# Kernel tuning notes

Measured on AMD Instinct MI355X. Metric: run time of the kernel, lower is better.

The kernel has to match this reference:

```python
import jax, jax.numpy as jnp
import numpy as np

OUT = 7            # output_size
SR = 2             # sampling_ratio
SCALES = (0.25, 0.125, 0.0625, 0.03125)  # P2..P5
CANON_S = 224.0
CANON_L = 4.0
LVL_EPS = 1e-6
K_MIN, K_MAX = 2, 5  # -log2(scales[0]), -log2(scales[-1])


def setup_inputs() -> dict:
    key = jax.random.key(0)
    ks = jax.random.split(key, 6)
    B, C, N = 2, 256, 256
    sizes = (200, 100, 50, 25)
    inp = {}
    for i, (k, hw) in enumerate(zip(ks[:4], sizes)):
        inp[f"feat{i}"] = jax.random.normal(k, (B, C, hw, hw), dtype=jnp.float32)
    x1y1 = jax.random.uniform(ks[4], (B, N, 2), minval=0.0, maxval=600.0)
    wh = jax.random.uniform(ks[5], (B, N, 2), minval=16.0, maxval=256.0)
    boxes = jnp.concatenate([x1y1, jnp.minimum(x1y1 + wh, 800.0)], axis=-1)
    inp["boxes"] = boxes.astype(jnp.float32)
    return inp


def _roi_align(feat, rois, scale):
    """torchvision RoIAlign (aligned=False). feat [B,C,H,W], rois [N,5] (bidx,x1,y1,x2,y2)."""
    B, C, H, W = feat.shape
    bidx = rois[:, 0].astype(jnp.int32)
    x1 = rois[:, 1] * scale
    y1 = rois[:, 2] * scale
    x2 = rois[:, 3] * scale
    y2 = rois[:, 4] * scale
    roi_w = jnp.maximum(x2 - x1, 1.0)
    roi_h = jnp.maximum(y2 - y1, 1.0)
    bin_h = roi_h / OUT
    bin_w = roi_w / OUT
    g = jnp.arange(OUT * SR)
    bin_idx = (g // SR).astype(feat.dtype)
    sub = (g % SR).astype(feat.dtype) + 0.5
    # sample coordinates [N, G] with G = OUT*SR
    ys = y1[:, None] + bin_idx * bin_h[:, None] + sub * bin_h[:, None] / SR
    xs = x1[:, None] + bin_idx * bin_w[:, None] + sub * bin_w[:, None] / SR
    vy = (ys >= -1.0) & (ys <= H)
    vx = (xs >= -1.0) & (xs <= W)
    y = jnp.clip(ys, 0.0, H - 1.0)
    x = jnp.clip(xs, 0.0, W - 1.0)
    y0 = jnp.floor(y).astype(jnp.int32)
    x0 = jnp.floor(x).astype(jnp.int32)
    y1i = jnp.minimum(y0 + 1, H - 1)
    x1i = jnp.minimum(x0 + 1, W - 1)
    ly = y - y0
    lx = x - x0
    hy = 1.0 - ly
    hx = 1.0 - lx

    def gather(yi, xi):
        # advanced indices at dims 0,2,3 with slice at dim 1 -> [N, G, G, C]
        return feat[bidx[:, None, None], :, yi[:, :, None], xi[:, None, :]]

    v = (gather(y0, x0) * (hy[:, :, None] * hx[:, None, :])[..., None]
         + gather(y0, x1i) * (hy[:, :, None] * lx[:, None, :])[..., None]
         + gather(y1i, x0) * (ly[:, :, None] * hx[:, None, :])[..., None]
         + gather(y1i, x1i) * (ly[:, :, None] * lx[:, None, :])[..., None])
    mask = (vy[:, :, None] & vx[:, None, :])[..., None]
    v = jnp.where(mask, v, 0.0)                       # [N, G, G, C]
    n = v.shape[0]
    v = v.reshape(n, OUT, SR, OUT, SR, C).mean(axis=(2, 4))  # avg pool per bin
    return jnp.transpose(v, (0, 3, 1, 2))             # [N, C, OUT, OUT]


def reference(feat0, feat1, feat2, feat3, boxes):
    feats = [feat0, feat1, feat2, feat3]
    B, N = boxes.shape[:2]
    flat = boxes.reshape(B * N, 4)
    ids = jnp.repeat(jnp.arange(B, dtype=flat.dtype), N)[:, None]
    rois = jnp.concatenate([ids, flat], axis=1)       # [B*N, 5]
    # FPN level assignment heuristic (LevelMapper)
    area = (flat[:, 2] - flat[:, 0]) * (flat[:, 3] - flat[:, 1])
    s = jnp.sqrt(area)
    lvl = jnp.floor(CANON_L + jnp.log2(s / CANON_S) + LVL_EPS)
    levels = jnp.clip(lvl, K_MIN, K_MAX).astype(jnp.int32) - K_MIN
    # Pool every roi at every level (static shapes), then select by level,
    # equivalent math to the gather/scatter-merge in the original.
    pooled = jnp.stack([_roi_align(f, rois, sc) for f, sc in zip(feats, SCALES)], axis=0)
    return pooled[levels, jnp.arange(B * N)]          # [B*N, C, OUT, OUT]
```

## Files before the change

### kernel.cpp

```cpp
#include <hip/hip_runtime.h>
#include <hip/hip_fp16.h>


#define ROI_OUT 7
#define NSAMP   14
#define C_TOT   256
#define N_PER_B 256
#define BINS    49
#define TOT_HW  53125

#define NTILE_X 832

__global__ __launch_bounds__(256)
void repack_kernel(const float* __restrict__ f0, const float* __restrict__ f1,
                   const float* __restrict__ f2, const float* __restrict__ f3,
                   __half* __restrict__ ws)
{
    __shared__ float tile[64][65];

    const int tx = blockIdx.x;
    const float* feat; int HW, base;
    int hw0;
    if (tx < 625)      { feat = f0; HW = 40000; base = 0;     hw0 = tx * 64; }
    else if (tx < 782) { feat = f1; HW = 10000; base = 40000; hw0 = (tx - 625) * 64; }
    else if (tx < 822) { feat = f2; HW = 2500;  base = 50000; hw0 = (tx - 782) * 64; }
    else               { feat = f3; HW = 625;   base = 52500; hw0 = (tx - 822) * 64; }

    const int c0 = blockIdx.y * 64;
    const int b  = blockIdx.z;
    const float* src = feat + (size_t)(b * C_TOT + c0) * (size_t)HW;

    const int hl  = threadIdx.x & 63;
    const int cl0 = threadIdx.x >> 6;
    const int hw  = hw0 + hl;
    if (hw < HW) {
        #pragma unroll
        for (int i = 0; i < 16; ++i) {
            int cl = cl0 + 4 * i;
            tile[cl][hl] = src[(size_t)cl * HW + hw];
        }
    }
    __syncthreads();

    __half* dst = ws + ((size_t)b * TOT_HW + base) * C_TOT + c0;
    const int co  = (threadIdx.x & 31) * 2;
    const int ho0 = threadIdx.x >> 5;
    #pragma unroll
    for (int i = 0; i < 8; ++i) {
        int ho  = ho0 + 8 * i;
        int hw2 = hw0 + ho;
        if (hw2 < HW) {
            __half2 v = __floats2half2_rn(tile[co][ho], tile[co + 1][ho]);
            *(__half2*)(dst + (size_t)hw2 * C_TOT + co) = v;
        }
    }
}

__global__ __launch_bounds__(256)
void msroi_main(const __half* __restrict__ ws, const float* __restrict__ boxes,
                float* __restrict__ out)
{
    __shared__ float oacc[C_TOT * BINS];
    __shared__ int4  pY[NSAMP], pX[NSAMP];

    const int tid = threadIdx.x;
    const int roi = blockIdx.x;
    const int b   = roi >> 8;

    const float* bxp = boxes + (size_t)roi * 4;
    float bx1 = bxp[0], by1 = bxp[1], bx2 = bxp[2], by2 = bxp[3];
    float area = (bx2 - bx1) * (by2 - by1);
    float s    = sqrtf(area);
    float lvlf = floorf(4.0f + log2f(s * (1.0f / 224.0f)) + 1e-6f);
    lvlf = fminf(fmaxf(lvlf, 2.0f), 5.0f);
    int level = (int)lvlf - 2;

    int H, W, lvbase; float scale;
    switch (level) {
        case 0:  H = 200; W = 200; lvbase = 0;     scale = 0.25f;    break;
        case 1:  H = 100; W = 100; lvbase = 40000; scale = 0.125f;   break;
        case 2:  H = 50;  W = 50;  lvbase = 50000; scale = 0.0625f;  break;
        default: H = 25;  W = 25;  lvbase = 52500; scale = 0.03125f; break;
    }

    float x1 = bx1 * scale, y1 = by1 * scale;
    float roi_w = fmaxf(bx2 * scale - x1, 1.0f);
    float roi_h = fmaxf(by2 * scale - y1, 1.0f);
    float bin_w = roi_w * (1.0f / ROI_OUT);
    float bin_h = roi_h * (1.0f / ROI_OUT);

    if (tid < 2 * NSAMP) {
        bool isy = tid >= NSAMP;
        int  j   = isy ? tid - NSAMP : tid;
        int  pb  = j >> 1, sub = j & 1;
        float start = isy ? y1 : x1;
        float bsz   = isy ? bin_h : bin_w;
        int   lim   = isy ? H : W;
        float ss = start + (float)pb * bsz + ((float)sub + 0.5f) * bsz * 0.5f;
        float v  = (ss >= -1.0f && ss <= (float)lim) ? 1.0f : 0.0f;
        float cc = fminf(fmaxf(ss, 0.0f), (float)lim - 1.0f);
        int   i0 = (int)floorf(cc);
        int   i1 = min(i0 + 1, lim - 1);
        float l  = cc - (float)i0;
        int4 pk; pk.x = i0; pk.y = i1;
        pk.z = __float_as_int(l); pk.w = __float_as_int(v);
        if (isy) pY[j] = pk; else pX[j] = pk;
    }
    __syncthreads();

    const int wave = tid >> 6;
    const int lane = tid & 63;
    const int c    = lane * 4;
    const __half* base = ws + ((size_t)b * TOT_HW + lvbase) * C_TOT + c;

    for (int bin = wave; bin < BINS; bin += 4) {
        int ph = bin / ROI_OUT;
        int pw = bin - ph * ROI_OUT;
        float a0 = 0.f, a1 = 0.f, a2 = 0.f, a3 = 0.f;

        #pragma unroll
        for (int sy = 0; sy < 2; ++sy) {
            int4 py  = pY[2 * ph + sy];
            float ly = __int_as_float(py.z);
            float vy = __int_as_float(py.w);
            float hy = 1.0f - ly;
            #pragma unroll
            for (int sx = 0; sx < 2; ++sx) {
                int4 px  = pX[2 * pw + sx];
                float lx = __int_as_float(px.z);
                float vv = vy * __int_as_float(px.w);
                float hx = 1.0f - lx;
                float w00 = vv * hy * hx, w01 = vv * hy * lx;
                float w10 = vv * ly * hx, w11 = vv * ly * lx;

                const __half2* p00 = (const __half2*)(base + (size_t)(py.x * W + px.x) * C_TOT);
                const __half2* p01 = (const __half2*)(base + (size_t)(py.x * W + px.y) * C_TOT);
                const __half2* p10 = (const __half2*)(base + (size_t)(py.y * W + px.x) * C_TOT);
                const __half2* p11 = (const __half2*)(base + (size_t)(py.y * W + px.y) * C_TOT);

                float2 g0, g1;
                g0 = __half22float2(p00[0]); g1 = __half22float2(p00[1]);
                a0 += w00 * g0.x; a1 += w00 * g0.y; a2 += w00 * g1.x; a3 += w00 * g1.y;
                g0 = __half22float2(p01[0]); g1 = __half22float2(p01[1]);
                a0 += w01 * g0.x; a1 += w01 * g0.y; a2 += w01 * g1.x; a3 += w01 * g1.y;
                g0 = __half22float2(p10[0]); g1 = __half22float2(p10[1]);
                a0 += w10 * g0.x; a1 += w10 * g0.y; a2 += w10 * g1.x; a3 += w10 * g1.y;
                g0 = __half22float2(p11[0]); g1 = __half22float2(p11[1]);
                a0 += w11 * g0.x; a1 += w11 * g0.y; a2 += w11 * g1.x; a3 += w11 * g1.y;
            }
        }
        oacc[(c + 0) * BINS + bin] = a0 * 0.25f;
        oacc[(c + 1) * BINS + bin] = a1 * 0.25f;
        oacc[(c + 2) * BINS + bin] = a2 * 0.25f;
        oacc[(c + 3) * BINS + bin] = a3 * 0.25f;
    }
    __syncthreads();

    float4*       o4 = (float4*)(out + (size_t)roi * (C_TOT * BINS));
    const float4* s4 = (const float4*)oacc;
    for (int j = tid; j < (C_TOT * BINS) / 4; j += 256) o4[j] = s4[j];
}

__global__ __launch_bounds__(256)
void msroi_direct(const float* __restrict__ f0, const float* __restrict__ f1,
                  const float* __restrict__ f2, const float* __restrict__ f3,
                  const float* __restrict__ boxes, float* __restrict__ out, int total)
{
    int e = blockIdx.x * 256 + threadIdx.x;
    if (e >= total) return;
    int bin = e % BINS;
    int c   = (e / BINS) % C_TOT;
    int roi = e / (BINS * C_TOT);
    int b   = roi / N_PER_B;

    const float* bx = boxes + (size_t)roi * 4;
    float bx1 = bx[0], by1 = bx[1], bx2 = bx[2], by2 = bx[3];
    float area = (bx2 - bx1) * (by2 - by1);
    float s    = sqrtf(area);
    float lvlf = floorf(4.0f + log2f(s * (1.0f / 224.0f)) + 1e-6f);
    lvlf = fminf(fmaxf(lvlf, 2.0f), 5.0f);
    int level = (int)lvlf - 2;

    const float* feat; int H, W; float scale;
    switch (level) {
        case 0:  feat = f0; H = 200; W = 200; scale = 0.25f;    break;
        case 1:  feat = f1; H = 100; W = 100; scale = 0.125f;   break;
        case 2:  feat = f2; H = 50;  W = 50;  scale = 0.0625f;  break;
        default: feat = f3; H = 25;  W = 25;  scale = 0.03125f; break;
    }
    float x1 = bx1 * scale, y1 = by1 * scale;
    float roi_w = fmaxf(bx2 * scale - x1, 1.0f);
    float roi_h = fmaxf(by2 * scale - y1, 1.0f);
    float bin_w = roi_w * (1.0f / ROI_OUT);
    float bin_h = roi_h * (1.0f / ROI_OUT);
    int ph = bin / ROI_OUT, pw = bin - ph * ROI_OUT;
    const float* plane = feat + ((size_t)(b * C_TOT + c)) * (size_t)(H * W);
    float Hf = (float)H, Wf = (float)W, acc = 0.0f;
    #pragma unroll
    for (int sy = 0; sy < 2; ++sy) {
        float ys = y1 + (float)ph * bin_h + ((float)sy + 0.5f) * bin_h * 0.5f;
        float vy = (ys >= -1.0f && ys <= Hf) ? 1.0f : 0.0f;
        float y  = fminf(fmaxf(ys, 0.0f), Hf - 1.0f);
        int   y0 = (int)floorf(y);
        int   y1i = min(y0 + 1, H - 1);
        float ly = y - (float)y0, hy = 1.0f - ly;
        int ro0 = y0 * W, ro1 = y1i * W;
        #pragma unroll
        for (int sx = 0; sx < 2; ++sx) {
            float xs = x1 + (float)pw * bin_w + ((float)sx + 0.5f) * bin_w * 0.5f;
            float vx = (xs >= -1.0f && xs <= Wf) ? 1.0f : 0.0f;
            float x  = fminf(fmaxf(xs, 0.0f), Wf - 1.0f);
            int   x0 = (int)floorf(x);
            int   x1i = min(x0 + 1, W - 1);
            float lx = x - (float)x0, hx = 1.0f - lx;
            float v00 = plane[ro0 + x0],  v01 = plane[ro0 + x1i];
            float v10 = plane[ro1 + x0],  v11 = plane[ro1 + x1i];
            acc += vy * vx * (hy * (hx * v00 + lx * v01) + ly * (hx * v10 + lx * v11));
        }
    }
    out[e] = acc * 0.25f;
}

extern "C" void kernel_launch(void* const* d_in, const int* in_sizes, int n_in,
                              void* d_out, int out_size, void* d_ws, size_t ws_size,
                              hipStream_t stream)
{
    const float* f0    = (const float*)d_in[0];
    const float* f1    = (const float*)d_in[1];
    const float* f2    = (const float*)d_in[2];
    const float* f3    = (const float*)d_in[3];
    const float* boxes = (const float*)d_in[4];
    float* out = (float*)d_out;

    const size_t ws_needed = (size_t)2 * TOT_HW * C_TOT * sizeof(__half);
    if (ws_size >= ws_needed) {
        __half* ws = (__half*)d_ws;
        hipLaunchKernelGGL(repack_kernel, dim3(NTILE_X, 4, 2), dim3(256), 0, stream,
                           f0, f1, f2, f3, ws);
        hipLaunchKernelGGL(msroi_main, dim3(2 * N_PER_B), dim3(256), 0, stream,
                           ws, boxes, out);
    } else {
        int total = out_size;
        hipLaunchKernelGGL(msroi_direct, dim3((total + 255) / 256), dim3(256), 0, stream,
                           f0, f1, f2, f3, boxes, out, total);
    }
}
```

Before: 48.57 us.

## Replace repack+gather with fused kernel staging per-ROI NCHW windows in LDS

Drops the NHWC fp16 repack pass over all feature maps and the two-kernel schedule. A single fused kernel instead has each block (ROI × 64-channel quarter) compute the ROI's sample bounding window and stage it into shared memory 8 channels at a time, straight from the NCHW fp32 inputs. Bilinear sampling then reads from LDS, with a direct global-memory fallback when the window exceeds 1024 elements. This removes the full-feature-map read/write of the repack. The cost is row-strided, partly uncoalesced window loads, many __syncthreads per channel tile, and only 392 of 512 threads doing compute.

```diff
diff --git a/kernel.cpp b/kernel.cpp
--- a/kernel.cpp
+++ b/kernel.cpp
@@ -1,5 +1,4 @@
 #include <hip/hip_runtime.h>
-#include <hip/hip_fp16.h>
 
 
 #define ROI_OUT 7
@@ -7,60 +6,18 @@
 #define C_TOT   256
 #define N_PER_B 256
 #define BINS    49
-#define TOT_HW  53125
+#define CT      8
+#define WCAP    1024
+#define WSTRIDE 1032
+#define THREADS 512
+#define CQ      64
 
-#define NTILE_X 832
-
-__global__ __launch_bounds__(256)
-void repack_kernel(const float* __restrict__ f0, const float* __restrict__ f1,
-                   const float* __restrict__ f2, const float* __restrict__ f3,
-                   __half* __restrict__ ws)
+__global__ __launch_bounds__(THREADS)
+void msroi_fused(const float* __restrict__ f0, const float* __restrict__ f1,
+                 const float* __restrict__ f2, const float* __restrict__ f3,
+                 const float* __restrict__ boxes, float* __restrict__ out)
 {
-    __shared__ float tile[64][65];
-
-    const int tx = blockIdx.x;
-    const float* feat; int HW, base;
-    int hw0;
-    if (tx < 625)      { feat = f0; HW = 40000; base = 0;     hw0 = tx * 64; }
-    else if (tx < 782) { feat = f1; HW = 10000; base = 40000; hw0 = (tx - 625) * 64; }
-    else if (tx < 822) { feat = f2; HW = 2500;  base = 50000; hw0 = (tx - 782) * 64; }
-    else               { feat = f3; HW = 625;   base = 52500; hw0 = (tx - 822) * 64; }
-
-    const int c0 = blockIdx.y * 64;
-    const int b  = blockIdx.z;
-    const float* src = feat + (size_t)(b * C_TOT + c0) * (size_t)HW;
-
-    const int hl  = threadIdx.x & 63;
-    const int cl0 = threadIdx.x >> 6;
-    const int hw  = hw0 + hl;
-    if (hw < HW) {
-        #pragma unroll
-        for (int i = 0; i < 16; ++i) {
-            int cl = cl0 + 4 * i;
-            tile[cl][hl] = src[(size_t)cl * HW + hw];
-        }
-    }
-    __syncthreads();
-
-    __half* dst = ws + ((size_t)b * TOT_HW + base) * C_TOT + c0;
-    const int co  = (threadIdx.x & 31) * 2;
-    const int ho0 = threadIdx.x >> 5;
-    #pragma unroll
-    for (int i = 0; i < 8; ++i) {
-        int ho  = ho0 + 8 * i;
-        int hw2 = hw0 + ho;
-        if (hw2 < HW) {
-            __half2 v = __floats2half2_rn(tile[co][ho], tile[co + 1][ho]);
-            *(__half2*)(dst + (size_t)hw2 * C_TOT + co) = v;
-        }
-    }
-}
-
-__global__ __launch_bounds__(256)
-void msroi_main(const __half* __restrict__ ws, const float* __restrict__ boxes,
-                float* __restrict__ out)
-{
-    __shared__ float oacc[C_TOT * BINS];
+    __shared__ float win[CT * WSTRIDE];
     __shared__ int4  pY[NSAMP], pX[NSAMP];
 
     const int tid = threadIdx.x;
@@ -75,13 +32,14 @@
     lvlf = fminf(fmaxf(lvlf, 2.0f), 5.0f);
     int level = (int)lvlf - 2;
 
-    int H, W, lvbase; float scale;
+    const float* feat; int H, W; float scale;
     switch (level) {
-        case 0:  H = 200; W = 200; lvbase = 0;     scale = 0.25f;    break;
-        case 1:  H = 100; W = 100; lvbase = 40000; scale = 0.125f;   break;
-        case 2:  H = 50;  W = 50;  lvbase = 50000; scale = 0.0625f;  break;
-        default: H = 25;  W = 25;  lvbase = 52500; scale = 0.03125f; break;
+        case 0:  feat = f0; H = 200; W = 200; scale = 0.25f;    break;
+        case 1:  feat = f1; H = 100; W = 100; scale = 0.125f;   break;
+        case 2:  feat = f2; H = 50;  W = 50;  scale = 0.0625f;  break;
+        default: feat = f3; H = 25;  W = 25;  scale = 0.03125f; break;
     }
+    const size_t HWsz = (size_t)H * (size_t)W;
 
     float x1 = bx1 * scale, y1 = by1 * scale;
     float roi_w = fmaxf(bx2 * scale - x1, 1.0f);
@@ -108,117 +66,95 @@
     }
     __syncthreads();
 
-    const int wave = tid >> 6;
-    const int lane = tid & 63;
-    const int c    = lane * 4;
-    const __half* base = ws + ((size_t)b * TOT_HW + lvbase) * C_TOT + c;
+    int ylo = 1 << 30, yhi = 0, xlo = 1 << 30, xhi = 0;
+    #pragma unroll
+    for (int j = 0; j < NSAMP; ++j) {
+        int4 py = pY[j]; int4 px = pX[j];
+        ylo = min(ylo, py.x); yhi = max(yhi, py.y);
+        xlo = min(xlo, px.x); xhi = max(xhi, px.y);
+    }
+    const int ny  = yhi - ylo + 1;
+    const int nx  = xhi - xlo + 1;
+    const int nyx = ny * nx;
+    const bool staged = (nyx <= WCAP);
 
-    for (int bin = wave; bin < BINS; bin += 4) {
-        int ph = bin / ROI_OUT;
-        int pw = bin - ph * ROI_OUT;
-        float a0 = 0.f, a1 = 0.f, a2 = 0.f, a3 = 0.f;
+    const float* fbase = feat + (size_t)b * C_TOT * HWsz;
+    float*       orow  = out + (size_t)roi * (C_TOT * BINS);
+    const int    cq0   = blockIdx.y * CQ;
 
-        #pragma unroll
-        for (int sy = 0; sy < 2; ++sy) {
-            int4 py  = pY[2 * ph + sy];
-            float ly = __int_as_float(py.z);
-            float vy = __int_as_float(py.w);
-            float hy = 1.0f - ly;
+    for (int tile = 0; tile < CQ / CT; ++tile) {
+        const int c0 = cq0 + tile * CT;
+
+        __syncthreads();
+        if (staged) {
             #pragma unroll
-            for (int sx = 0; sx < 2; ++sx) {
-                int4 px  = pX[2 * pw + sx];
-                float lx = __int_as_float(px.z);
-                float vv = vy * __int_as_float(px.w);
-                float hx = 1.0f - lx;
-                float w00 = vv * hy * hx, w01 = vv * hy * lx;
-                float w10 = vv * ly * hx, w11 = vv * ly * lx;
-
-                const __half2* p00 = (const __half2*)(base + (size_t)(py.x * W + px.x) * C_TOT);
-                const __half2* p01 = (const __half2*)(base + (size_t)(py.x * W + px.y) * C_TOT);
-                const __half2* p10 = (const __half2*)(base + (size_t)(py.y * W + px.x) * C_TOT);
-                const __half2* p11 = (const __half2*)(base + (size_t)(py.y * W + px.y) * C_TOT);
-
-                float2 g0, g1;
-                g0 = __half22float2(p00[0]); g1 = __half22float2(p00[1]);
-                a0 += w00 * g0.x; a1 += w00 * g0.y; a2 += w00 * g1.x; a3 += w00 * g1.y;
-                g0 = __half22float2(p01[0]); g1 = __half22float2(p01[1]);
-                a0 += w01 * g0.x; a1 += w01 * g0.y; a2 += w01 * g1.x; a3 += w01 * g1.y;
-                g0 = __half22float2(p10[0]); g1 = __half22float2(p10[1]);
-                a0 += w10 * g0.x; a1 += w10 * g0.y; a2 += w10 * g1.x; a3 += w10 * g1.y;
-                g0 = __half22float2(p11[0]); g1 = __half22float2(p11[1]);
-                a0 += w11 * g0.x; a1 += w11 * g0.y; a2 += w11 * g1.x; a3 += w11 * g1.y;
+            for (int cl = 0; cl < CT; ++cl) {
+                const float* pl = fbase + (size_t)(c0 + cl) * HWsz;
+                float* wb = win + cl * WSTRIDE;
+                for (unsigned j = tid; j < (unsigned)nyx; j += THREADS) {
+                    unsigned yy = j / (unsigned)nx;
+                    unsigned xx = j - yy * (unsigned)nx;
+                    wb[j] = pl[(size_t)(ylo + (int)yy) * W + xlo + (int)xx];
+                }
             }
         }
-        oacc[(c + 0) * BINS + bin] = a0 * 0.25f;
-        oacc[(c + 1) * BINS + bin] = a1 * 0.25f;
-        oacc[(c + 2) * BINS + bin] = a2 * 0.25f;
-        oacc[(c + 3) * BINS + bin] = a3 * 0.25f;
-    }
-    __syncthreads();
+        __syncthreads();
 
-    float4*       o4 = (float4*)(out + (size_t)roi * (C_TOT * BINS));
-    const float4* s4 = (const float4*)oacc;
-    for (int j = tid; j < (C_TOT * BINS) / 4; j += 256) o4[j] = s4[j];
-}
+        if (tid < CT * BINS) {
+            int cl  = tid / BINS;
+            int bin = tid - cl * BINS;
+            int ph  = bin / ROI_OUT;
+            int pw  = bin - ph * ROI_OUT;
+            float acc = 0.0f;
 
-__global__ __launch_bounds__(256)
-void msroi_direct(const float* __restrict__ f0, const float* __restrict__ f1,
-                  const float* __restrict__ f2, const float* __restrict__ f3,
-                  const float* __restrict__ boxes, float* __restrict__ out, int total)
-{
-    int e = blockIdx.x * 256 + threadIdx.x;
-    if (e >= total) return;
-    int bin = e % BINS;
-    int c   = (e / BINS) % C_TOT;
-    int roi = e / (BINS * C_TOT);
-    int b   = roi / N_PER_B;
-
-    const float* bx = boxes + (size_t)roi * 4;
-    float bx1 = bx[0], by1 = bx[1], bx2 = bx[2], by2 = bx[3];
-    float area = (bx2 - bx1) * (by2 - by1);
-    float s    = sqrtf(area);
-    float lvlf = floorf(4.0f + log2f(s * (1.0f / 224.0f)) + 1e-6f);
-    lvlf = fminf(fmaxf(lvlf, 2.0f), 5.0f);
-    int level = (int)lvlf - 2;
-
-    const float* feat; int H, W; float scale;
-    switch (level) {
-        case 0:  feat = f0; H = 200; W = 200; scale = 0.25f;    break;
-        case 1:  feat = f1; H = 100; W = 100; scale = 0.125f;   break;
-        case 2:  feat = f2; H = 50;  W = 50;  scale = 0.0625f;  break;
-        default: feat = f3; H = 25;  W = 25;  scale = 0.03125f; break;
-    }
-    float x1 = bx1 * scale, y1 = by1 * scale;
-    float roi_w = fmaxf(bx2 * scale - x1, 1.0f);
-    float roi_h = fmaxf(by2 * scale - y1, 1.0f);
-    float bin_w = roi_w * (1.0f / ROI_OUT);
-    float bin_h = roi_h * (1.0f / ROI_OUT);
-    int ph = bin / ROI_OUT, pw = bin - ph * ROI_OUT;
-    const float* plane = feat + ((size_t)(b * C_TOT + c)) * (size_t)(H * W);
-    float Hf = (float)H, Wf = (float)W, acc = 0.0f;
-    #pragma unroll
-    for (int sy = 0; sy < 2; ++sy) {
-        float ys = y1 + (float)ph * bin_h + ((float)sy + 0.5f) * bin_h * 0.5f;
-        float vy = (ys >= -1.0f && ys <= Hf) ? 1.0f : 0.0f;
-        float y  = fminf(fmaxf(ys, 0.0f), Hf - 1.0f);
-        int   y0 = (int)floorf(y);
-        int   y1i = min(y0 + 1, H - 1);
-        float ly = y - (float)y0, hy = 1.0f - ly;
-        int ro0 = y0 * W, ro1 = y1i * W;
-        #pragma unroll
-        for (int sx = 0; sx < 2; ++sx) {
-            float xs = x1 + (float)pw * bin_w + ((float)sx + 0.5f) * bin_w * 0.5f;
-            float vx = (xs >= -1.0f && xs <= Wf) ? 1.0f : 0.0f;
-            float x  = fminf(fmaxf(xs, 0.0f), Wf - 1.0f);
-            int   x0 = (int)floorf(x);
-            int   x1i = min(x0 + 1, W - 1);
-            float lx = x - (float)x0, hx = 1.0f - lx;
-            float v00 = plane[ro0 + x0],  v01 = plane[ro0 + x1i];
-            float v10 = plane[ro1 + x0],  v11 = plane[ro1 + x1i];
-            acc += vy * vx * (hy * (hx * v00 + lx * v01) + ly * (hx * v10 + lx * v11));
+            if (staged) {
+                const float* wb = win + cl * WSTRIDE;
+                #pragma unroll
+                for (int sy = 0; sy < 2; ++sy) {
+                    int4 py  = pY[2 * ph + sy];
+                    float ly = __int_as_float(py.z);
+                    float vy = __int_as_float(py.w);
+                    float hy = 1.0f - ly;
+                    int r0 = (py.x - ylo) * nx - xlo;
+                    int r1 = (py.y - ylo) * nx - xlo;
+                    #pragma unroll
+                    for (int sx = 0; sx < 2; ++sx) {
+                        int4 px  = pX[2 * pw + sx];
+                        float lx = __int_as_float(px.z);
+                        float vv = vy * __int_as_float(px.w);
+                        float hx = 1.0f - lx;
+                        float v00 = wb[r0 + px.x], v01 = wb[r0 + px.y];
+                        float v10 = wb[r1 + px.x], v11 = wb[r1 + px.y];
+                        acc += vv * (hy * (hx * v00 + lx * v01)
+                                   + ly * (hx * v10 + lx * v11));
+                    }
+                }
+            } else {
+                const float* pl = fbase + (size_t)(c0 + cl) * HWsz;
+                #pragma unroll
+                for (int sy = 0; sy < 2; ++sy) {
+                    int4 py  = pY[2 * ph + sy];
+                    float ly = __int_as_float(py.z);
+                    float vy = __int_as_float(py.w);
+                    float hy = 1.0f - ly;
+                    const float* r0 = pl + (size_t)py.x * W;
+                    const float* r1 = pl + (size_t)py.y * W;
+                    #pragma unroll
+                    for (int sx = 0; sx < 2; ++sx) {
+                        int4 px  = pX[2 * pw + sx];
+                        float lx = __int_as_float(px.z);
+                        float vv = vy * __int_as_float(px.w);
+                        float hx = 1.0f - lx;
+                        float v00 = r0[px.x], v01 = r0[px.y];
+                        float v10 = r1[px.x], v11 = r1[px.y];
+                        acc += vv * (hy * (hx * v00 + lx * v01)
+                                   + ly * (hx * v10 + lx * v11));
+                    }
+                }
+            }
+            orow[(size_t)(c0 + cl) * BINS + bin] = acc * 0.25f;
         }
     }
-    out[e] = acc * 0.25f;
 }
 
 extern "C" void kernel_launch(void* const* d_in, const int* in_sizes, int n_in,
@@ -232,16 +168,6 @@
     const float* boxes = (const float*)d_in[4];
     float* out = (float*)d_out;
 
-    const size_t ws_needed = (size_t)2 * TOT_HW * C_TOT * sizeof(__half);
-    if (ws_size >= ws_needed) {
-        __half* ws = (__half*)d_ws;
-        hipLaunchKernelGGL(repack_kernel, dim3(NTILE_X, 4, 2), dim3(256), 0, stream,
-                           f0, f1, f2, f3, ws);
-        hipLaunchKernelGGL(msroi_main, dim3(2 * N_PER_B), dim3(256), 0, stream,
-                           ws, boxes, out);
-    } else {
-        int total = out_size;
-        hipLaunchKernelGGL(msroi_direct, dim3((total + 255) / 256), dim3(256), 0, stream,
-                           f0, f1, f2, f3, boxes, out, total);
-    }
+    hipLaunchKernelGGL(msroi_fused, dim3(2 * N_PER_B, C_TOT / CQ), dim3(THREADS),
+                       0, stream, f0, f1, f2, f3, boxes, out);
 }
```

New measurement: 159.7 us. 229% more time.
